# Kernel optimization log

Hardware: AMD Instinct MI355X
Metric: run time of the kernel (lower is better)

Reference implementation:

```python
import jax, jax.numpy as jnp
import numpy as np

B, S, H, P = 64, 2048, 1024, 8
MIN_BITS, MAX_BITS = 2.0, 8.0


def setup_inputs() -> dict:
    key = jax.random.key(0)
    k1, k2, k3 = jax.random.split(key, 3)
    return {
        "hidden_states": jax.random.normal(k1, (B, S, H), dtype=jnp.float32),
        "W1": 0.02 * jax.random.normal(k2, (H, H), dtype=jnp.float32),  # torch Linear: (out,in)
        "b1": jnp.zeros((H,), dtype=jnp.float32),
        "W2": 0.02 * jax.random.normal(k3, (P, H), dtype=jnp.float32),
        "b2": jnp.zeros((P,), dtype=jnp.float32),
        "temperature": jnp.ones((1,), dtype=jnp.float32),
        "total_budget": 32,
    }


def reference(hidden_states, W1, b1, W2, b2, temperature, total_budget):
    budget = jnp.float32(total_budget)
    # mean-pool over sequence: (B,S,H) -> (B,H); this dominates memory traffic
    pooled = hidden_states.mean(axis=1)
    h = jax.nn.silu(pooled @ W1.T + b1)          # (B,H)
    logits = h @ W2.T + b2                        # (B,P)
    temp = jnp.clip(temperature, 0.1, 5.0)
    attn_probs = jax.nn.softmax(logits / temp, axis=-1)
    # continuous bit allocation
    x = jnp.clip(attn_probs * budget, MIN_BITS, MAX_BITS)
    x = x * (budget / (x.sum(axis=-1, keepdims=True) + 1e-8))
    # straight-through round
    bits = jnp.round(x) - jax.lax.stop_gradient(x) + x  # numerically round(x)
    # vectorized exact-budget correction (torch loops per-sample with .item() syncs)
    diff = jax.lax.stop_gradient(jnp.trunc(budget - bits.sum(axis=-1)))  # (B,) int-valued, int() truncation
    idx = jnp.where(diff > 0, jnp.argmax(bits, axis=-1), jnp.argmin(bits, axis=-1))
    rows = jnp.arange(bits.shape[0])
    cur = bits[rows, idx]
    new = jnp.clip(cur + diff, MIN_BITS, MAX_BITS)
    bits = bits.at[rows, idx].set(jnp.where(diff != 0, new, cur))
    return bits, attn_probs
```

## Files before the change

### kernel.cpp

```cpp
#include <hip/hip_runtime.h>
#include <math.h>

#define BB 64
#define SS 2048
#define HH 1024
#define PP 8
#define SPLIT 32
#define ROWS (SS / SPLIT)

typedef float vf4 __attribute__((ext_vector_type(4)));

__global__ __launch_bounds__(256) void pool_partial_k(const float* __restrict__ hs,
                                                      float* __restrict__ part) {
    int blk = blockIdx.x;
    int b  = blk / SPLIT;
    int sp = blk % SPLIT;
    int t  = threadIdx.x;
    const vf4* base = reinterpret_cast<const vf4*>(
        hs + (size_t)b * SS * HH + (size_t)sp * ROWS * HH);
    vf4 acc0 = (vf4)0.f;
    vf4 acc1 = (vf4)0.f;
    #pragma unroll 4
    for (int s = 0; s < ROWS; s += 2) {
        vf4 v0 = __builtin_nontemporal_load(&base[(size_t)s * (HH / 4) + t]);
        vf4 v1 = __builtin_nontemporal_load(&base[(size_t)(s + 1) * (HH / 4) + t]);
        acc0 += v0;
        acc1 += v1;
    }
    vf4 acc = acc0 + acc1;
    reinterpret_cast<vf4*>(part)[(size_t)blk * (HH / 4) + t] = acc;
}

__global__ __launch_bounds__(256) void pool_finish_k(const float* __restrict__ part,
                                                     float* __restrict__ pooled) {
    int idx = blockIdx.x * 256 + threadIdx.x;
    int b = idx >> 8;
    int c = idx & 255;
    const vf4* p4 = reinterpret_cast<const vf4*>(part);
    vf4 s = (vf4)0.f;
    #pragma unroll
    for (int sp = 0; sp < SPLIT; ++sp)
        s += p4[((size_t)b * SPLIT + sp) * (HH / 4) + c];
    s *= (1.0f / (float)SS);
    reinterpret_cast<vf4*>(pooled)[idx] = s;
}

__global__ __launch_bounds__(256) void gemm1_silu_k(const float* __restrict__ pooled,
                                                    const float* __restrict__ W1,
                                                    const float* __restrict__ b1,
                                                    float* __restrict__ hbuf) {
    int b  = blockIdx.x >> 4;
    int oc = blockIdx.x & 15;
    int t  = threadIdx.x;
    int wave = t >> 6, lane = t & 63;
    __shared__ vf4 spool[HH / 4];
    spool[t] = reinterpret_cast<const vf4*>(pooled + (size_t)b * HH)[t];
    __syncthreads();
    int obase = oc * 64 + wave * 16;
    float myz = 0.f;
    for (int j = 0; j < 16; ++j) {
        const vf4* wrow = reinterpret_cast<const vf4*>(W1 + (size_t)(obase + j) * HH);
        float s = 0.f;
        #pragma unroll
        for (int k = 0; k < 4; ++k) {
            vf4 wv = wrow[lane + 64 * k];
            vf4 pv = spool[lane + 64 * k];
            s += wv.x * pv.x + wv.y * pv.y + wv.z * pv.z + wv.w * pv.w;
        }
        #pragma unroll
        for (int off = 32; off; off >>= 1) s += __shfl_xor(s, off);
        if (lane == j) myz = s;
    }
    if (lane < 16) {
        int o = obase + lane;
        float z = myz + b1[o];
        hbuf[(size_t)b * HH + o] = z / (1.f + expf(-z));
    }
}

__global__ __launch_bounds__(256) void head_k(const float* __restrict__ hbuf,
                                              const float* __restrict__ W2,
                                              const float* __restrict__ b2,
                                              const float* __restrict__ temp_p,
                                              const int* __restrict__ budget_p,
                                              float* __restrict__ out) {
    int b = blockIdx.x;
    int t = threadIdx.x;
    int wave = t >> 6, lane = t & 63;
    __shared__ float slog[PP];

    {
        const vf4* hrow = reinterpret_cast<const vf4*>(hbuf + (size_t)b * HH);
        int p0 = wave * 2, p1 = wave * 2 + 1;
        const vf4* w0 = reinterpret_cast<const vf4*>(W2 + (size_t)p0 * HH);
        const vf4* w1 = reinterpret_cast<const vf4*>(W2 + (size_t)p1 * HH);
        float s0 = 0.f, s1 = 0.f;
        #pragma unroll
        for (int k = 0; k < 4; ++k) {
            vf4 hv = hrow[lane + 64 * k];
            vf4 a = w0[lane + 64 * k];
            vf4 c = w1[lane + 64 * k];
            s0 += a.x * hv.x + a.y * hv.y + a.z * hv.z + a.w * hv.w;
            s1 += c.x * hv.x + c.y * hv.y + c.z * hv.z + c.w * hv.w;
        }
        #pragma unroll
        for (int off = 32; off; off >>= 1) {
            s0 += __shfl_xor(s0, off);
            s1 += __shfl_xor(s1, off);
        }
        if (lane == 0) {
            slog[p0] = s0 + b2[p0];
            slog[p1] = s1 + b2[p1];
        }
    }
    __syncthreads();
    if (wave != 0) return;

    float logit[PP];
    #pragma unroll
    for (int p = 0; p < PP; ++p) logit[p] = slog[p];
    float temp = fminf(fmaxf(temp_p[0], 0.1f), 5.0f);
    float budget = (float)budget_p[0];
    float inv_t = 1.0f / temp;
    float m = -INFINITY;
    #pragma unroll
    for (int p = 0; p < PP; ++p) { logit[p] *= inv_t; m = fmaxf(m, logit[p]); }
    float e[PP], se = 0.f;
    #pragma unroll
    for (int p = 0; p < PP; ++p) { e[p] = expf(logit[p] - m); se += e[p]; }
    float probs[PP];
    float inv_se = 1.0f / se;
    #pragma unroll
    for (int p = 0; p < PP; ++p) probs[p] = e[p] * inv_se;

    float x[PP], sx = 0.f;
    #pragma unroll
    for (int p = 0; p < PP; ++p) {
        x[p] = fminf(fmaxf(probs[p] * budget, 2.0f), 8.0f);
        sx += x[p];
    }
    float r = budget / (sx + 1e-8f);
    float bits[PP], sb = 0.f;
    #pragma unroll
    for (int p = 0; p < PP; ++p) {
        x[p] *= r;
        bits[p] = rintf(x[p]);
        sb += bits[p];
    }
    float diff = truncf(budget - sb);
    if (diff != 0.f) {
        int idx = 0;
        if (diff > 0.f) {
            float best = bits[0];
            for (int p = 1; p < PP; ++p) if (bits[p] > best) { best = bits[p]; idx = p; }
        } else {
            float best = bits[0];
            for (int p = 1; p < PP; ++p) if (bits[p] < best) { best = bits[p]; idx = p; }
        }
        bits[idx] = fminf(fmaxf(bits[idx] + diff, 2.0f), 8.0f);
    }

    int lane0 = t;
    if (lane0 < PP)            out[b * PP + lane0] = bits[lane0];
    else if (lane0 < 2 * PP)   out[BB * PP + b * PP + (lane0 - PP)] = probs[lane0 - PP];
}

extern "C" void kernel_launch(void* const* d_in, const int* in_sizes, int n_in,
                              void* d_out, int out_size, void* d_ws, size_t ws_size,
                              hipStream_t stream) {
    const float* hs     = (const float*)d_in[0];
    const float* W1     = (const float*)d_in[1];
    const float* b1     = (const float*)d_in[2];
    const float* W2     = (const float*)d_in[3];
    const float* b2     = (const float*)d_in[4];
    const float* temp   = (const float*)d_in[5];
    const int*   budget = (const int*)d_in[6];
    float* out = (float*)d_out;

    float* ws     = (float*)d_ws;
    float* part   = ws;
    float* pooled = ws + (size_t)BB * SPLIT * HH;
    float* hbuf   = pooled + (size_t)BB * HH;

    hipLaunchKernelGGL(pool_partial_k, dim3(BB * SPLIT), dim3(256), 0, stream, hs, part);
    hipLaunchKernelGGL(pool_finish_k,  dim3(BB * HH / 4 / 256), dim3(256), 0, stream, part, pooled);
    hipLaunchKernelGGL(gemm1_silu_k,   dim3(BB * 16), dim3(256), 0, stream, pooled, W1, b1, hbuf);
    hipLaunchKernelGGL(head_k,         dim3(BB), dim3(256), 0, stream, hbuf, W2, b2, temp, budget, out);
}
```

Measured before the change: 106.6 us.

## Fuse pool finish into GEMM1 and batch four rows per W1 load

Removes the separate pool-finish kernel. The GEMM1 kernel now reduces the split partial sums itself into shared memory for four batch rows, then computes dot products for those four rows from each loaded W1 row, so W1 traffic drops by four. SPLIT is halved to 16, which shrinks the partial buffer and the reduction work but launches fewer blocks for the dominant pooling pass. The fused kernel uses 512-thread blocks and 256 blocks, and each block repeats the partial reduction for its 4 rows across the 16 output chunks.

```diff
diff --git a/kernel.cpp b/kernel.cpp
--- a/kernel.cpp
+++ b/kernel.cpp
@@ -5,7 +5,7 @@
 #define SS 2048
 #define HH 1024
 #define PP 8
-#define SPLIT 32
+#define SPLIT 16
 #define ROWS (SS / SPLIT)
 
 typedef float vf4 __attribute__((ext_vector_type(4)));
@@ -27,54 +27,69 @@
         acc0 += v0;
         acc1 += v1;
     }
-    vf4 acc = acc0 + acc1;
-    reinterpret_cast<vf4*>(part)[(size_t)blk * (HH / 4) + t] = acc;
-}
-
-__global__ __launch_bounds__(256) void pool_finish_k(const float* __restrict__ part,
-                                                     float* __restrict__ pooled) {
-    int idx = blockIdx.x * 256 + threadIdx.x;
-    int b = idx >> 8;
-    int c = idx & 255;
-    const vf4* p4 = reinterpret_cast<const vf4*>(part);
-    vf4 s = (vf4)0.f;
-    #pragma unroll
-    for (int sp = 0; sp < SPLIT; ++sp)
-        s += p4[((size_t)b * SPLIT + sp) * (HH / 4) + c];
-    s *= (1.0f / (float)SS);
-    reinterpret_cast<vf4*>(pooled)[idx] = s;
-}
-
-__global__ __launch_bounds__(256) void gemm1_silu_k(const float* __restrict__ pooled,
+    reinterpret_cast<vf4*>(part)[(size_t)blk * (HH / 4) + t] = acc0 + acc1;
+}
+
+__global__ __launch_bounds__(512) void gemm_fused_k(const float* __restrict__ part,
                                                     const float* __restrict__ W1,
                                                     const float* __restrict__ b1,
                                                     float* __restrict__ hbuf) {
-    int b  = blockIdx.x >> 4;
+    int bg = blockIdx.x >> 4;
     int oc = blockIdx.x & 15;
     int t  = threadIdx.x;
     int wave = t >> 6, lane = t & 63;
-    __shared__ vf4 spool[HH / 4];
-    spool[t] = reinterpret_cast<const vf4*>(pooled + (size_t)b * HH)[t];
+    __shared__ vf4 spool[4][HH / 4];
+
+    {
+        int c  = t & 255;
+        int r0 = t >> 8;
+        #pragma unroll
+        for (int rr = 0; rr < 2; ++rr) {
+            int r = r0 + 2 * rr;
+            int b = bg * 4 + r;
+            const vf4* pb = reinterpret_cast<const vf4*>(part) +
+                            (size_t)b * SPLIT * (HH / 4) + c;
+            vf4 s = (vf4)0.f;
+            #pragma unroll
+            for (int sp = 0; sp < SPLIT; ++sp)
+                s += pb[(size_t)sp * (HH / 4)];
+            spool[r][c] = s * (1.0f / (float)SS);
+        }
+    }
     __syncthreads();
-    int obase = oc * 64 + wave * 16;
-    float myz = 0.f;
-    for (int j = 0; j < 16; ++j) {
-        const vf4* wrow = reinterpret_cast<const vf4*>(W1 + (size_t)(obase + j) * HH);
-        float s = 0.f;
-        #pragma unroll
-        for (int k = 0; k < 4; ++k) {
-            vf4 wv = wrow[lane + 64 * k];
-            vf4 pv = spool[lane + 64 * k];
-            s += wv.x * pv.x + wv.y * pv.y + wv.z * pv.z + wv.w * pv.w;
-        }
-        #pragma unroll
-        for (int off = 32; off; off >>= 1) s += __shfl_xor(s, off);
-        if (lane == j) myz = s;
-    }
-    if (lane < 16) {
-        int o = obase + lane;
-        float z = myz + b1[o];
-        hbuf[(size_t)b * HH + o] = z / (1.f + expf(-z));
+
+    int g = lane >> 4;
+    int q = lane & 15;
+    #pragma unroll
+    for (int i = 0; i < 2; ++i) {
+        int o = oc * 64 + wave * 8 + i * 4 + g;
+        const vf4* wrow = reinterpret_cast<const vf4*>(W1 + (size_t)o * HH);
+        float s0 = 0.f, s1 = 0.f, s2 = 0.f, s3 = 0.f;
+        #pragma unroll
+        for (int k = 0; k < 16; ++k) {
+            vf4 wv = wrow[q + 16 * k];
+            vf4 p0 = spool[0][q + 16 * k];
+            vf4 p1 = spool[1][q + 16 * k];
+            vf4 p2 = spool[2][q + 16 * k];
+            vf4 p3 = spool[3][q + 16 * k];
+            s0 += wv.x * p0.x + wv.y * p0.y + wv.z * p0.z + wv.w * p0.w;
+            s1 += wv.x * p1.x + wv.y * p1.y + wv.z * p1.z + wv.w * p1.w;
+            s2 += wv.x * p2.x + wv.y * p2.y + wv.z * p2.z + wv.w * p2.w;
+            s3 += wv.x * p3.x + wv.y * p3.y + wv.z * p3.z + wv.w * p3.w;
+        }
+        #pragma unroll
+        for (int off = 1; off < 16; off <<= 1) {
+            s0 += __shfl_xor(s0, off);
+            s1 += __shfl_xor(s1, off);
+            s2 += __shfl_xor(s2, off);
+            s3 += __shfl_xor(s3, off);
+        }
+        if (q < 4) {
+            float s = (q == 0) ? s0 : ((q == 1) ? s1 : ((q == 2) ? s2 : s3));
+            int b = bg * 4 + q;
+            float z = s + b1[o];
+            hbuf[(size_t)b * HH + o] = z / (1.f + expf(-z));
+        }
     }
 }
 
@@ -160,9 +175,8 @@
         bits[idx] = fminf(fmaxf(bits[idx] + diff, 2.0f), 8.0f);
     }
 
-    int lane0 = t;
-    if (lane0 < PP)            out[b * PP + lane0] = bits[lane0];
-    else if (lane0 < 2 * PP)   out[BB * PP + b * PP + (lane0 - PP)] = probs[lane0 - PP];
+    if (t < PP)            out[b * PP + t] = bits[t];
+    else if (t < 2 * PP)   out[BB * PP + b * PP + (t - PP)] = probs[t - PP];
 }
 
 extern "C" void kernel_launch(void* const* d_in, const int* in_sizes, int n_in,
@@ -177,13 +191,11 @@
     const int*   budget = (const int*)d_in[6];
     float* out = (float*)d_out;
 
-    float* ws     = (float*)d_ws;
-    float* part   = ws;
-    float* pooled = ws + (size_t)BB * SPLIT * HH;
-    float* hbuf   = pooled + (size_t)BB * HH;
+    float* ws   = (float*)d_ws;
+    float* part = ws;
+    float* hbuf = ws + (size_t)BB * SPLIT * HH;
 
     hipLaunchKernelGGL(pool_partial_k, dim3(BB * SPLIT), dim3(256), 0, stream, hs, part);
-    hipLaunchKernelGGL(pool_finish_k,  dim3(BB * HH / 4 / 256), dim3(256), 0, stream, part, pooled);
-    hipLaunchKernelGGL(gemm1_silu_k,   dim3(BB * 16), dim3(256), 0, stream, pooled, W1, b1, hbuf);
+    hipLaunchKernelGGL(gemm_fused_k,   dim3(256), dim3(512), 0, stream, part, W1, b1, hbuf);
     hipLaunchKernelGGL(head_k,         dim3(BB), dim3(256), 0, stream, hbuf, W2, b2, temp, budget, out);
 }
```

After: 102.6 us. 1.04x faster.
